# Performance work log

Hardware: AMD Instinct MI355X
Metric: run time of the kernel (lower is better)

## Reference

```python
import jax, jax.numpy as jnp
import numpy as np

INPUT_DIM = 256
EMBED_DIM = 256
NUM_HEADS = 8
HEAD_DIM = EMBED_DIM // NUM_HEADS
N_TOKENS = 11136
N_BATCH = 16


def _xavier(key, shape):
    fan_out, fan_in = shape
    bound = np.sqrt(6.0 / (fan_in + fan_out)).astype(np.float32)
    return jax.random.uniform(key, shape, jnp.float32, -bound, bound)


def setup_inputs() -> dict:
    key = jax.random.key(0)
    k_x, k_ids, k_qkv, k_o = jax.random.split(key, 4)
    x = jax.random.normal(k_x, (N_TOKENS, INPUT_DIM), jnp.float32)
    batch_ids = jnp.sort(jax.random.randint(k_ids, (N_TOKENS,), 0, N_BATCH)).astype(jnp.int32)
    qkv_w = _xavier(k_qkv, (3 * EMBED_DIM, INPUT_DIM))
    qkv_b = jnp.zeros((3 * EMBED_DIM,), jnp.float32)
    o_w = _xavier(k_o, (EMBED_DIM, EMBED_DIM))
    o_b = jnp.zeros((EMBED_DIM,), jnp.float32)
    return {"x": x, "batch_ids": batch_ids, "qkv_w": qkv_w, "qkv_b": qkv_b,
            "o_w": o_w, "o_b": o_b}


def reference(x, batch_ids, qkv_w, qkv_b, o_w, o_b):
    # batch_ids is concrete metadata (mirrors np.unique on CPU in the original).
    ids = np.asarray(batch_ids)
    vals, counts = np.unique(ids, return_counts=True)
    B = len(vals)
    S = int(counts.max())
    offsets = np.concatenate([np.zeros(1, np.int64), np.cumsum(counts)[:-1]])
    seg = np.searchsorted(vals, ids)               # segment index per token
    pos = np.arange(ids.shape[0]) - offsets[seg]   # position within segment

    qkv = x @ qkv_w.T + qkv_b                      # [N, 3E]
    # pad_sequence with padding_value=1 -> scatter tokens into an all-ones buffer
    fin = jnp.ones((B, S, 3 * EMBED_DIM), qkv.dtype).at[seg, pos].set(qkv)
    # padded rows sum to exactly 3E (all ones) -> mask True marks padding
    pad_mask = fin.sum(-1) >= fin.shape[-1]        # [B, S]

    qkv4 = fin.reshape(B, S, NUM_HEADS, 3 * HEAD_DIM).transpose(0, 2, 1, 3)
    q, k, v = jnp.split(qkv4, 3, axis=-1)          # each [B, H, S, hd]

    logits = jnp.einsum('bhqd,bhkd->bhqk', q, k) * (HEAD_DIM ** -0.5)
    logits = jnp.where(pad_mask[:, None, None, :], -jnp.inf, logits)
    attn = jax.nn.softmax(logits, axis=-1)         # [B, H, S, S]

    out = jnp.einsum('bhqk,bhkd->bhqd', attn, v)
    out = out.transpose(0, 2, 1, 3).reshape(B, S, EMBED_DIM)
    out = out[seg, pos]                            # unpad -> [N, E]
    return out @ o_w.T + o_b
```

## Files before the change

### kernel.cpp

```cpp
#include <hip/hip_runtime.h>
#include <stdint.h>


#define N_TOK 11136
#define E 256
#define H 8
#define HD 32

typedef __attribute__((ext_vector_type(8))) __bf16 bf16x8;
typedef __attribute__((ext_vector_type(8))) unsigned short u16x8;
typedef __attribute__((ext_vector_type(4))) float f32x4;

__device__ __forceinline__ unsigned short f2bf(float f) {
  unsigned int u = __float_as_uint(f);
  u = (u + 0x7FFFu + ((u >> 16) & 1u)) >> 16;
  return (unsigned short)u;
}
__device__ __forceinline__ float bf2f(unsigned short s) {
  return __uint_as_float(((unsigned int)s) << 16);
}
__device__ __forceinline__ bf16x8 ld8(const unsigned short* p) {
  return *(const bf16x8*)p;
}
__device__ __forceinline__ unsigned int cvtpk(float a, float b) {
  unsigned int r;
  asm("v_cvt_pk_bf16_f32 %0, %1, %2" : "=v"(r) : "v"(a), "v"(b));
  return r;
}

__global__ void k_split(const float* __restrict__ x, const float* __restrict__ qw,
                        const float* __restrict__ ow, const int* __restrict__ ids,
                        unsigned short* __restrict__ xhi, unsigned short* __restrict__ xlo,
                        unsigned short* __restrict__ whi, unsigned short* __restrict__ wlo,
                        unsigned short* __restrict__ owb, int* __restrict__ offs) {
  if (blockIdx.x == 0 && threadIdx.x < 17) {
    int b = threadIdx.x, lo = 0, hi = N_TOK;
    while (lo < hi) { int mid = (lo + hi) >> 1; if (ids[mid] < b) lo = mid + 1; else hi = mid; }
    offs[b] = lo;
  }
  const int NX4 = N_TOK * E / 4;
  const int NW4 = 3 * E * E / 4;
  const int NO4 = E * E / 4;
  int total = NX4 + NW4 + NO4;
  for (int i = blockIdx.x * blockDim.x + threadIdx.x; i < total;
       i += gridDim.x * blockDim.x) {
    if (i < NX4) {
      float4 v = ((const float4*)x)[i];
      ushort4 hv, lv;
      hv.x = f2bf(v.x); lv.x = f2bf(v.x - bf2f(hv.x));
      hv.y = f2bf(v.y); lv.y = f2bf(v.y - bf2f(hv.y));
      hv.z = f2bf(v.z); lv.z = f2bf(v.z - bf2f(hv.z));
      hv.w = f2bf(v.w); lv.w = f2bf(v.w - bf2f(hv.w));
      ((ushort4*)xhi)[i] = hv; ((ushort4*)xlo)[i] = lv;
    } else if (i < NX4 + NW4) {
      int j = i - NX4;
      float4 v = ((const float4*)qw)[j];
      ushort4 hv, lv;
      hv.x = f2bf(v.x); lv.x = f2bf(v.x - bf2f(hv.x));
      hv.y = f2bf(v.y); lv.y = f2bf(v.y - bf2f(hv.y));
      hv.z = f2bf(v.z); lv.z = f2bf(v.z - bf2f(hv.z));
      hv.w = f2bf(v.w); lv.w = f2bf(v.w - bf2f(hv.w));
      ((ushort4*)whi)[j] = hv; ((ushort4*)wlo)[j] = lv;
    } else {
      int j = i - NX4 - NW4;
      float4 v = ((const float4*)ow)[j];
      ushort4 hv;
      hv.x = f2bf(v.x); hv.y = f2bf(v.y); hv.z = f2bf(v.z); hv.w = f2bf(v.w);
      ((ushort4*)owb)[j] = hv;
    }
  }
}

#define QK_BSTRIDE 264
#define QSCALE (0.17677669529663687f * 1.4426950408889634f)
__global__ __launch_bounds__(256, 3) void k_qkv(
    const unsigned short* __restrict__ xhi, const unsigned short* __restrict__ xlo,
    const unsigned short* __restrict__ whi, const unsigned short* __restrict__ wlo,
    const float* __restrict__ qkv_b,
    unsigned short* __restrict__ Qb, unsigned short* __restrict__ Kb,
    unsigned short* __restrict__ Vt) {
  int bid = blockIdx.x + 16 * blockIdx.y;
  int xcd = bid & 7;
  int j8 = bid >> 3;
  int colb = j8 & 15;
  int tile = (j8 >> 4) * 8 + xcd;
  if (tile >= 58) return;
  int col0 = colb * 48;
  __shared__ __align__(16) unsigned short Bhi[48 * QK_BSTRIDE];
  __shared__ __align__(16) unsigned short Blo[48 * QK_BSTRIDE];
  int tid = threadIdx.x;
  int w = tid >> 6, lane = tid & 63, m = lane & 15, quad = lane >> 4;
  int rowb = tile * 192 + w * 48;

  {
    const u16x8* wh8 = (const u16x8*)(whi + (size_t)col0 * E);
    const u16x8* wl8 = (const u16x8*)(wlo + (size_t)col0 * E);
#pragma unroll
    for (int i = 0; i < 6; ++i) {
      int flat = i * 256 + tid;
      int row = flat >> 5, c8 = flat & 31;
      *(u16x8*)(Bhi + row * QK_BSTRIDE + c8 * 8) = wh8[flat];
      *(u16x8*)(Blo + row * QK_BSTRIDE + c8 * 8) = wl8[flat];
    }
  }
  __syncthreads();

  f32x4 acc[3][3] = {};
  bf16x8 ah1[3], al1[3], ah2[3], al2[3];
#pragma unroll
  for (int mt = 0; mt < 3; ++mt) {
    const size_t ro = (size_t)(rowb + mt * 16 + m) * E + quad * 8;
    ah1[mt] = ld8(xhi + ro);       al1[mt] = ld8(xlo + ro);
    ah2[mt] = ld8(xhi + ro + 32);  al2[mt] = ld8(xlo + ro + 32);
  }
  for (int kc = 0; kc < 8; ++kc) {
    bf16x8 ah[3], al[3];
#pragma unroll
    for (int mt = 0; mt < 3; ++mt) {
      ah[mt] = ah1[mt]; al[mt] = al1[mt];
      ah1[mt] = ah2[mt]; al1[mt] = al2[mt];
    }
    int kn = kc + 2; if (kn > 7) kn = 7;
    int kon = kn * 32 + quad * 8;
#pragma unroll
    for (int mt = 0; mt < 3; ++mt) {
      const size_t ro = (size_t)(rowb + mt * 16 + m) * E + kon;
      ah2[mt] = ld8(xhi + ro);
      al2[mt] = ld8(xlo + ro);
    }
    int ko = kc * 32 + quad * 8;
#pragma unroll
    for (int t = 0; t < 3; ++t) {
      bf16x8 bh = ld8(Bhi + (16 * t + m) * QK_BSTRIDE + ko);
      bf16x8 bl = ld8(Blo + (16 * t + m) * QK_BSTRIDE + ko);
#pragma unroll
      for (int mt = 0; mt < 3; ++mt) {
        acc[mt][t] = __builtin_amdgcn_mfma_f32_16x16x32_bf16(ah[mt], bh, acc[mt][t], 0, 0, 0);
        acc[mt][t] = __builtin_amdgcn_mfma_f32_16x16x32_bf16(ah[mt], bl, acc[mt][t], 0, 0, 0);
        acc[mt][t] = __builtin_amdgcn_mfma_f32_16x16x32_bf16(al[mt], bh, acc[mt][t], 0, 0, 0);
      }
    }
  }
#pragma unroll
  for (int t = 0; t < 3; ++t) {
    int j = col0 + 16 * t + m;
    int hd = j / 96;
    int rr = j - hd * 96;
    float bias = qkv_b[j];
#pragma unroll
    for (int mt = 0; mt < 3; ++mt) {
      int tokb = rowb + mt * 16 + quad * 4;
      if (rr < 64) {
        float qsc = (rr < 32) ? QSCALE : 1.0f;
        unsigned short* dst = (rr < 32) ? (Qb + (size_t)hd * N_TOK * HD + rr)
                                        : (Kb + (size_t)hd * N_TOK * HD + (rr - 32));
#pragma unroll
        for (int r = 0; r < 4; ++r)
          dst[(size_t)(tokb + r) * HD] = f2bf((acc[mt][t][r] + bias) * qsc);
      } else {
        int d = rr - 64;
        ushort4 pk;
        pk.x = f2bf(acc[mt][t][0] + bias); pk.y = f2bf(acc[mt][t][1] + bias);
        pk.z = f2bf(acc[mt][t][2] + bias); pk.w = f2bf(acc[mt][t][3] + bias);
        *(ushort4*)(Vt + (size_t)(hd * HD + d) * N_TOK + tokb) = pk;
      }
    }
  }
}

#define PSTRIDE 72
#define VSTR 72
__global__ __launch_bounds__(128, 3) void k_attn(
    const int* __restrict__ ids, const int* __restrict__ offs,
    const unsigned short* __restrict__ Qb, const unsigned short* __restrict__ Kb,
    const unsigned short* __restrict__ Vt,
    unsigned short* __restrict__ attnb) {
  __shared__ __align__(16) unsigned short Kl[2][64 * 32];
  __shared__ __align__(16) unsigned short Vl[2][32 * VSTR];
  __shared__ __align__(16) unsigned short ldsP[2][32 * PSTRIDE];
  __shared__ int bred[4];
  int tid = threadIdx.x;
  int w = tid >> 6, lane = tid & 63;
  int m = lane & 15, quad = lane >> 4;
  int h = blockIdx.x;
  int tok0 = blockIdx.y * 64;
  int q0 = tok0 + w * 32;
  unsigned short* P = ldsP[w];
  int tA = q0 + m;
  int tB = q0 + 16 + m;
  int bA = ids[tA], bB = ids[tB];
  int st0 = offs[bA], en0 = offs[bA + 1];
  int st1 = offs[bB], en1 = offs[bB + 1];
  int kmin = min(st0, st1), kmax = max(en0, en1);
  int stM = max(st0, st1), enm = min(en0, en1);
#pragma unroll
  for (int d = 1; d <= 8; d <<= 1) {
    kmin = min(kmin, __shfl_xor(kmin, d));
    kmax = max(kmax, __shfl_xor(kmax, d));
    stM  = max(stM,  __shfl_xor(stM,  d));
    enm  = min(enm,  __shfl_xor(enm,  d));
  }
  if (lane == 0) { bred[w] = kmin; bred[2 + w] = kmax; }
  __syncthreads();
  int kminB = min(bred[0], bred[1]);
  int kmaxB = max(bred[2], bred[3]);
  int k0beg = kminB & ~63;

  const unsigned short* Kbase = Kb + (size_t)h * N_TOK * HD;
  const unsigned short* Vbase = Vt + (size_t)h * HD * N_TOK;
  bf16x8 qf0 = ld8(Qb + (size_t)(h * N_TOK + tA) * HD + quad * 8);
  bf16x8 qf1 = ld8(Qb + (size_t)(h * N_TOK + tB) * HD + quad * 8);

  int kr = tid >> 2;
  int kgof = (tid & 3) * 8;
  int vr = tid >> 3;
  int vgof = (tid & 7) * 8;

  bf16x8 kgA = ld8(Kbase + (size_t)(k0beg + kr) * HD + kgof);
  bf16x8 kgB = ld8(Kbase + (size_t)(k0beg + 32 + kr) * HD + kgof);
  bf16x8 vgA = ld8(Vbase + (size_t)vr * N_TOK + k0beg + vgof);
  bf16x8 vgB = ld8(Vbase + (size_t)(16 + vr) * N_TOK + k0beg + vgof);
  *(bf16x8*)(&Kl[0][kr * 32 + kgof]) = kgA;
  *(bf16x8*)(&Kl[0][(32 + kr) * 32 + kgof]) = kgB;
  *(bf16x8*)(&Vl[0][vr * VSTR + vgof]) = vgA;
  *(bf16x8*)(&Vl[0][(16 + vr) * VSTR + vgof]) = vgB;
  __syncthreads();

  float lsum0 = 0.f, lsum1 = 0.f;
  f32x4 o00 = {}, o01 = {}, o10 = {}, o11 = {};
  int buf = 0;
  for (int k0 = k0beg; k0 < kmaxB; k0 += 64) {
    int k1 = (k0 + 64 < kmaxB) ? (k0 + 64) : k0;
    kgA = ld8(Kbase + (size_t)(k1 + kr) * HD + kgof);
    kgB = ld8(Kbase + (size_t)(k1 + 32 + kr) * HD + kgof);
    vgA = ld8(Vbase + (size_t)vr * N_TOK + k1 + vgof);
    vgB = ld8(Vbase + (size_t)(16 + vr) * N_TOK + k1 + vgof);
    const unsigned short* Kc = &Kl[buf][0];
    const unsigned short* Vc = &Vl[buf][0];
    f32x4 s0[4], s1[4];
    __builtin_amdgcn_s_setprio(1);
#pragma unroll
    for (int i = 0; i < 4; ++i) {
      bf16x8 kf = ld8(Kc + (16 * i + m) * 32 + quad * 8);
      f32x4 z = {};
      s0[i] = __builtin_amdgcn_mfma_f32_16x16x32_bf16(kf, qf0, z, 0, 0, 0);
      f32x4 z2 = {};
      s1[i] = __builtin_amdgcn_mfma_f32_16x16x32_bf16(kf, qf1, z2, 0, 0, 0);
    }
    __builtin_amdgcn_s_setprio(0);
    bool interior = (k0 >= stM && k0 + 64 <= enm);
    int jb = k0 + quad * 4;
#pragma unroll
    for (int i = 0; i < 4; ++i) {
      float p0[4], p1[4];
#pragma unroll
      for (int r = 0; r < 4; ++r) {
        float sv0 = s0[i][r], sv1 = s1[i][r];
        if (!interior) {
          int j = jb + 16 * i + r;
          sv0 = (j >= st0 && j < en0) ? sv0 : -3e38f;
          sv1 = (j >= st1 && j < en1) ? sv1 : -3e38f;
        }
        float e0, e1;
        asm("v_exp_f32 %0, %1" : "=v"(e0) : "v"(sv0));
        asm("v_exp_f32 %0, %1" : "=v"(e1) : "v"(sv1));
        p0[r] = e0; p1[r] = e1;
      }
      lsum0 += (p0[0] + p0[1]) + (p0[2] + p0[3]);
      lsum1 += (p1[0] + p1[1]) + (p1[2] + p1[3]);
      uint2 pk0, pk1;
      pk0.x = cvtpk(p0[0], p0[1]); pk0.y = cvtpk(p0[2], p0[3]);
      pk1.x = cvtpk(p1[0], p1[1]); pk1.y = cvtpk(p1[2], p1[3]);
      *(uint2*)(P + m * PSTRIDE + 16 * i + quad * 4) = pk0;
      *(uint2*)(P + (16 + m) * PSTRIDE + 16 * i + quad * 4) = pk1;
    }
    __builtin_amdgcn_s_setprio(1);
#pragma unroll
    for (int c = 0; c < 2; ++c) {
      bf16x8 vf0 = ld8(Vc + m * VSTR + 32 * c + quad * 8);
      bf16x8 vf1 = ld8(Vc + (16 + m) * VSTR + 32 * c + quad * 8);
      bf16x8 pf0 = ld8(P + m * PSTRIDE + 32 * c + quad * 8);
      bf16x8 pf1 = ld8(P + (16 + m) * PSTRIDE + 32 * c + quad * 8);
      o00 = __builtin_amdgcn_mfma_f32_16x16x32_bf16(vf0, pf0, o00, 0, 0, 0);
      o01 = __builtin_amdgcn_mfma_f32_16x16x32_bf16(vf1, pf0, o01, 0, 0, 0);
      o10 = __builtin_amdgcn_mfma_f32_16x16x32_bf16(vf0, pf1, o10, 0, 0, 0);
      o11 = __builtin_amdgcn_mfma_f32_16x16x32_bf16(vf1, pf1, o11, 0, 0, 0);
    }
    __builtin_amdgcn_s_setprio(0);
    *(bf16x8*)(&Kl[buf ^ 1][kr * 32 + kgof]) = kgA;
    *(bf16x8*)(&Kl[buf ^ 1][(32 + kr) * 32 + kgof]) = kgB;
    *(bf16x8*)(&Vl[buf ^ 1][vr * VSTR + vgof]) = vgA;
    *(bf16x8*)(&Vl[buf ^ 1][(16 + vr) * VSTR + vgof]) = vgB;
    __syncthreads();
    buf ^= 1;
  }
  lsum0 += __shfl_xor(lsum0, 16);
  lsum0 += __shfl_xor(lsum0, 32);
  lsum1 += __shfl_xor(lsum1, 16);
  lsum1 += __shfl_xor(lsum1, 32);
  float inv0 = 1.0f / lsum0;
  float inv1 = 1.0f / lsum1;
  uint2 w00, w01, w10, w11;
  w00.x = cvtpk(o00[0] * inv0, o00[1] * inv0);
  w00.y = cvtpk(o00[2] * inv0, o00[3] * inv0);
  w01.x = cvtpk(o01[0] * inv0, o01[1] * inv0);
  w01.y = cvtpk(o01[2] * inv0, o01[3] * inv0);
  w10.x = cvtpk(o10[0] * inv1, o10[1] * inv1);
  w10.y = cvtpk(o10[2] * inv1, o10[3] * inv1);
  w11.x = cvtpk(o11[0] * inv1, o11[1] * inv1);
  w11.y = cvtpk(o11[2] * inv1, o11[3] * inv1);
  *(uint2*)(attnb + (size_t)tA * E + h * HD + quad * 4) = w00;
  *(uint2*)(attnb + (size_t)tA * E + h * HD + 16 + quad * 4) = w01;
  *(uint2*)(attnb + (size_t)tB * E + h * HD + quad * 4) = w10;
  *(uint2*)(attnb + (size_t)tB * E + h * HD + 16 + quad * 4) = w11;
}

__global__ __launch_bounds__(256, 4) void k_oproj(
    const unsigned short* __restrict__ attnb, const unsigned short* __restrict__ owb,
    const float* __restrict__ ob, float* __restrict__ out) {
  __shared__ __align__(16) unsigned short Bo[64 * QK_BSTRIDE];
  int tid = threadIdx.x;
  int w = tid >> 6, lane = tid & 63, m = lane & 15, quad = lane >> 4;
  int tok0 = blockIdx.x * 64, col0 = blockIdx.y * 64;
  {
    const u16x8* o8 = (const u16x8*)(owb + (size_t)col0 * E);
#pragma unroll
    for (int i = 0; i < 8; ++i) {
      int flat = i * 256 + tid;
      int row = flat >> 5, c8 = flat & 31;
      *(u16x8*)(Bo + row * QK_BSTRIDE + c8 * 8) = o8[flat];
    }
  }
  __syncthreads();
  f32x4 acc[4] = {};
  int arow = tok0 + 16 * w + m;
  const unsigned short* abase = attnb + (size_t)arow * E + quad * 8;
  bf16x8 a1 = ld8(abase);
  bf16x8 a2 = ld8(abase + 32);
  for (int kc = 0; kc < 8; ++kc) {
    bf16x8 a = a1;
    a1 = a2;
    int kn = kc + 2; if (kn > 7) kn = 7;
    a2 = ld8(abase + kn * 32);
    int ko = kc * 32 + quad * 8;
#pragma unroll
    for (int t = 0; t < 4; ++t) {
      bf16x8 b = ld8(Bo + (16 * t + m) * QK_BSTRIDE + ko);
      acc[t] = __builtin_amdgcn_mfma_f32_16x16x32_bf16(a, b, acc[t], 0, 0, 0);
    }
  }
#pragma unroll
  for (int t = 0; t < 4; ++t) {
    int j = col0 + 16 * t + m;
    float bias = ob[j];
#pragma unroll
    for (int r = 0; r < 4; ++r) {
      int tok = tok0 + 16 * w + quad * 4 + r;
      out[(size_t)tok * E + j] = acc[t][r] + bias;
    }
  }
}

extern "C" void kernel_launch(void* const* d_in, const int* in_sizes, int n_in,
                              void* d_out, int out_size, void* d_ws, size_t ws_size,
                              hipStream_t stream) {
  const float* x   = (const float*)d_in[0];
  const int*   ids = (const int*)d_in[1];
  const float* qw  = (const float*)d_in[2];
  const float* qb  = (const float*)d_in[3];
  const float* ow  = (const float*)d_in[4];
  const float* ob  = (const float*)d_in[5];
  float* out = (float*)d_out;

  char* p = (char*)d_ws;
  auto alloc = [&](size_t bytes) {
    char* r = p;
    p += (bytes + 255) & ~(size_t)255;
    return r;
  };
  int* offs = (int*)alloc(32 * sizeof(int));
  unsigned short* xhi = (unsigned short*)alloc((size_t)N_TOK * E * 2);
  unsigned short* xlo = (unsigned short*)alloc((size_t)N_TOK * E * 2);
  unsigned short* whi = (unsigned short*)alloc((size_t)3 * E * E * 2);
  unsigned short* wlo = (unsigned short*)alloc((size_t)3 * E * E * 2);
  unsigned short* owb = (unsigned short*)alloc((size_t)E * E * 2);
  unsigned short* Qb  = (unsigned short*)alloc((size_t)N_TOK * E * 2);
  unsigned short* Kb  = (unsigned short*)alloc((size_t)N_TOK * E * 2);
  unsigned short* Vt  = (unsigned short*)alloc((size_t)N_TOK * E * 2);
  unsigned short* att = (unsigned short*)alloc((size_t)N_TOK * E * 2);

  k_split<<<dim3(1712), dim3(256), 0, stream>>>(x, qw, ow, ids, xhi, xlo, whi, wlo, owb, offs);
  k_qkv<<<dim3(16, 64), dim3(256), 0, stream>>>(xhi, xlo, whi, wlo, qb, Qb, Kb, Vt);
  k_attn<<<dim3(H, N_TOK / 64), dim3(128), 0, stream>>>(ids, offs, Qb, Kb, Vt, att);
  k_oproj<<<dim3(N_TOK / 64, E / 64), dim3(256), 0, stream>>>(att, owb, ob, out);
}
```

Before: 157.5 us.

## Load K/V fragments directly from global into registers, drop LDS staging and barriers

Each wave now loads its own K and V MFMA operand fragments straight from global memory into registers, with a one-tile register prefetch, instead of cooperatively staging them in double-buffered LDS. Each wave also uses its own key range rather than the block-wide range, so the block barriers and the shared reduction go away. The intent is to remove LDS traffic and __syncthreads stalls. In exchange both waves of a block fetch the same K/V tiles separately, the loads are less coalesced, register pressure rises, and launch bounds drop from 3 to 2 blocks per unit.

```diff
diff --git a/kernel.cpp b/kernel.cpp
--- a/kernel.cpp
+++ b/kernel.cpp
@@ -169,16 +169,12 @@
 }
 
 #define PSTRIDE 72
-#define VSTR 72
-__global__ __launch_bounds__(128, 3) void k_attn(
+__global__ __launch_bounds__(128, 2) void k_attn(
     const int* __restrict__ ids, const int* __restrict__ offs,
     const unsigned short* __restrict__ Qb, const unsigned short* __restrict__ Kb,
     const unsigned short* __restrict__ Vt,
     unsigned short* __restrict__ attnb) {
-  __shared__ __align__(16) unsigned short Kl[2][64 * 32];
-  __shared__ __align__(16) unsigned short Vl[2][32 * VSTR];
   __shared__ __align__(16) unsigned short ldsP[2][32 * PSTRIDE];
-  __shared__ int bred[4];
   int tid = threadIdx.x;
   int w = tid >> 6, lane = tid & 63;
   int m = lane & 15, quad = lane >> 4;
@@ -200,52 +196,50 @@
     stM  = max(stM,  __shfl_xor(stM,  d));
     enm  = min(enm,  __shfl_xor(enm,  d));
   }
-  if (lane == 0) { bred[w] = kmin; bred[2 + w] = kmax; }
-  __syncthreads();
-  int kminB = min(bred[0], bred[1]);
-  int kmaxB = max(bred[2], bred[3]);
-  int k0beg = kminB & ~63;
+  int k0beg = kmin & ~63;
 
   const unsigned short* Kbase = Kb + (size_t)h * N_TOK * HD;
   const unsigned short* Vbase = Vt + (size_t)h * HD * N_TOK;
   bf16x8 qf0 = ld8(Qb + (size_t)(h * N_TOK + tA) * HD + quad * 8);
   bf16x8 qf1 = ld8(Qb + (size_t)(h * N_TOK + tB) * HD + quad * 8);
 
-  int kr = tid >> 2;
-  int kgof = (tid & 3) * 8;
-  int vr = tid >> 3;
-  int vgof = (tid & 7) * 8;
-
-  bf16x8 kgA = ld8(Kbase + (size_t)(k0beg + kr) * HD + kgof);
-  bf16x8 kgB = ld8(Kbase + (size_t)(k0beg + 32 + kr) * HD + kgof);
-  bf16x8 vgA = ld8(Vbase + (size_t)vr * N_TOK + k0beg + vgof);
-  bf16x8 vgB = ld8(Vbase + (size_t)(16 + vr) * N_TOK + k0beg + vgof);
-  *(bf16x8*)(&Kl[0][kr * 32 + kgof]) = kgA;
-  *(bf16x8*)(&Kl[0][(32 + kr) * 32 + kgof]) = kgB;
-  *(bf16x8*)(&Vl[0][vr * VSTR + vgof]) = vgA;
-  *(bf16x8*)(&Vl[0][(16 + vr) * VSTR + vgof]) = vgB;
-  __syncthreads();
+  const unsigned short* Kp  = Kbase + (size_t)m * HD + quad * 8;
+  const unsigned short* Vp0 = Vbase + (size_t)m * N_TOK + quad * 8;
+  const unsigned short* Vp1 = Vbase + (size_t)(16 + m) * N_TOK + quad * 8;
+
+  bf16x8 kfn[4], vfn0[2], vfn1[2];
+#pragma unroll
+  for (int i = 0; i < 4; ++i) kfn[i] = ld8(Kp + (size_t)(k0beg + 16 * i) * HD);
+#pragma unroll
+  for (int c = 0; c < 2; ++c) {
+    vfn0[c] = ld8(Vp0 + k0beg + 32 * c);
+    vfn1[c] = ld8(Vp1 + k0beg + 32 * c);
+  }
 
   float lsum0 = 0.f, lsum1 = 0.f;
   f32x4 o00 = {}, o01 = {}, o10 = {}, o11 = {};
-  int buf = 0;
-  for (int k0 = k0beg; k0 < kmaxB; k0 += 64) {
-    int k1 = (k0 + 64 < kmaxB) ? (k0 + 64) : k0;
-    kgA = ld8(Kbase + (size_t)(k1 + kr) * HD + kgof);
-    kgB = ld8(Kbase + (size_t)(k1 + 32 + kr) * HD + kgof);
-    vgA = ld8(Vbase + (size_t)vr * N_TOK + k1 + vgof);
-    vgB = ld8(Vbase + (size_t)(16 + vr) * N_TOK + k1 + vgof);
-    const unsigned short* Kc = &Kl[buf][0];
-    const unsigned short* Vc = &Vl[buf][0];
+  for (int k0 = k0beg; k0 < kmax; k0 += 64) {
+    bf16x8 kf[4], vf0[2], vf1[2];
+#pragma unroll
+    for (int i = 0; i < 4; ++i) kf[i] = kfn[i];
+#pragma unroll
+    for (int c = 0; c < 2; ++c) { vf0[c] = vfn0[c]; vf1[c] = vfn1[c]; }
+    int k1 = (k0 + 64 < kmax) ? (k0 + 64) : k0;
+#pragma unroll
+    for (int i = 0; i < 4; ++i) kfn[i] = ld8(Kp + (size_t)(k1 + 16 * i) * HD);
+#pragma unroll
+    for (int c = 0; c < 2; ++c) {
+      vfn0[c] = ld8(Vp0 + k1 + 32 * c);
+      vfn1[c] = ld8(Vp1 + k1 + 32 * c);
+    }
     f32x4 s0[4], s1[4];
     __builtin_amdgcn_s_setprio(1);
 #pragma unroll
     for (int i = 0; i < 4; ++i) {
-      bf16x8 kf = ld8(Kc + (16 * i + m) * 32 + quad * 8);
       f32x4 z = {};
-      s0[i] = __builtin_amdgcn_mfma_f32_16x16x32_bf16(kf, qf0, z, 0, 0, 0);
+      s0[i] = __builtin_amdgcn_mfma_f32_16x16x32_bf16(kf[i], qf0, z, 0, 0, 0);
       f32x4 z2 = {};
-      s1[i] = __builtin_amdgcn_mfma_f32_16x16x32_bf16(kf, qf1, z2, 0, 0, 0);
+      s1[i] = __builtin_amdgcn_mfma_f32_16x16x32_bf16(kf[i], qf1, z2, 0, 0, 0);
     }
     __builtin_amdgcn_s_setprio(0);
     bool interior = (k0 >= stM && k0 + 64 <= enm);
@@ -277,22 +271,14 @@
     __builtin_amdgcn_s_setprio(1);
 #pragma unroll
     for (int c = 0; c < 2; ++c) {
-      bf16x8 vf0 = ld8(Vc + m * VSTR + 32 * c + quad * 8);
-      bf16x8 vf1 = ld8(Vc + (16 + m) * VSTR + 32 * c + quad * 8);
       bf16x8 pf0 = ld8(P + m * PSTRIDE + 32 * c + quad * 8);
       bf16x8 pf1 = ld8(P + (16 + m) * PSTRIDE + 32 * c + quad * 8);
-      o00 = __builtin_amdgcn_mfma_f32_16x16x32_bf16(vf0, pf0, o00, 0, 0, 0);
-      o01 = __builtin_amdgcn_mfma_f32_16x16x32_bf16(vf1, pf0, o01, 0, 0, 0);
-      o10 = __builtin_amdgcn_mfma_f32_16x16x32_bf16(vf0, pf1, o10, 0, 0, 0);
-      o11 = __builtin_amdgcn_mfma_f32_16x16x32_bf16(vf1, pf1, o11, 0, 0, 0);
+      o00 = __builtin_amdgcn_mfma_f32_16x16x32_bf16(vf0[c], pf0, o00, 0, 0, 0);
+      o01 = __builtin_amdgcn_mfma_f32_16x16x32_bf16(vf1[c], pf0, o01, 0, 0, 0);
+      o10 = __builtin_amdgcn_mfma_f32_16x16x32_bf16(vf0[c], pf1, o10, 0, 0, 0);
+      o11 = __builtin_amdgcn_mfma_f32_16x16x32_bf16(vf1[c], pf1, o11, 0, 0, 0);
     }
     __builtin_amdgcn_s_setprio(0);
-    *(bf16x8*)(&Kl[buf ^ 1][kr * 32 + kgof]) = kgA;
-    *(bf16x8*)(&Kl[buf ^ 1][(32 + kr) * 32 + kgof]) = kgB;
-    *(bf16x8*)(&Vl[buf ^ 1][vr * VSTR + vgof]) = vgA;
-    *(bf16x8*)(&Vl[buf ^ 1][(16 + vr) * VSTR + vgof]) = vgB;
-    __syncthreads();
-    buf ^= 1;
   }
   lsum0 += __shfl_xor(lsum0, 16);
   lsum0 += __shfl_xor(lsum0, 32);
```

Measured after the change: 163.5 us. 1.04x slower.
